# Optimization experiments

Measured on AMD Instinct MI355X. Metric: run time of the kernel, lower is better.

Reference implementation:

```python
import jax, jax.numpy as jnp
import numpy as np

N = 20000
E = 320000
IN_F = 128
HEADS = 8
OUT_F = 32
NEG_SLOPE = 0.2


def setup_inputs() -> dict:
    key = jax.random.key(0)
    k = jax.random.split(key, 8)
    x = jax.random.normal(k[0], (N, IN_F), dtype=jnp.float32)
    edge_index = jax.random.randint(k[1], (2, E), 0, N, dtype=jnp.int32)
    # Linear weights stored torch-style: [out, in]
    scale = 1.0 / np.sqrt(IN_F)
    W = jax.random.normal(k[2], (HEADS * OUT_F, IN_F), dtype=jnp.float32) * scale
    W1 = jax.random.normal(k[3], (HEADS * OUT_F, IN_F), dtype=jnp.float32) * scale
    W2 = jax.random.normal(k[4], (HEADS * OUT_F, IN_F), dtype=jnp.float32) * scale
    att = jax.random.normal(k[5], (1, HEADS, OUT_F), dtype=jnp.float32) * 0.1
    bias = jnp.zeros((HEADS * OUT_F,), dtype=jnp.float32)
    return {"x": x, "edge_index": edge_index, "W": W, "W1": W1, "W2": W2,
            "att": att, "bias": bias}


def reference(x, edge_index, W, W1, W2, att, bias):
    n, heads, out_f = x.shape[0], att.shape[1], att.shape[2]
    src, dst = edge_index[0], edge_index[1]

    # Node projections: [N, H, F]
    h_src = (x @ W1.T).reshape(n, heads, out_f)
    h_dst = (x @ W2.T).reshape(n, heads, out_f)
    values = (x @ W.T).reshape(n, heads, out_f)

    # Edge-wise GATv2 logits: a^T LeakyReLU(W1 h_i + W2 h_j)  -> [E, H]
    att_input = jax.nn.leaky_relu(h_src[src] + h_dst[dst], negative_slope=NEG_SLOPE)
    logits = jnp.einsum('ehf,hf->eh', att_input, att[0])

    # Segment softmax over incoming edges of each dst node (stable).
    seg_max = jax.ops.segment_max(logits, dst, num_segments=n)  # [N, H]
    exp_l = jnp.exp(logits - seg_max[dst])
    denom = jax.ops.segment_sum(exp_l, dst, num_segments=n)     # [N, H]
    weights = exp_l / denom[dst]                                # [E, H]

    # Weighted aggregation of source values into dst nodes.
    weighted = weights[:, :, None] * values[src]                # [E, H, F]
    out = jax.ops.segment_sum(weighted, dst, num_segments=n)    # [N, H, F]

    out = out.reshape(n, heads * out_f) + bias
    return out
```

## Files before the change

kernel.cpp:

```cpp
#include <hip/hip_runtime.h>
#include <math.h>

#define NN 20000
#define EE 320000
#define KF 128
#define HO 256
#define CAP 96

typedef __attribute__((ext_vector_type(8))) short short8;
typedef __attribute__((ext_vector_type(4))) float f32x4;
typedef __attribute__((ext_vector_type(2))) _Float16 half2_t;

static __device__ __forceinline__ unsigned short f2bf(float f) {
    union { float f; unsigned u; } v; v.f = f;
    unsigned u = v.u;
    u += 0x7fffu + ((u >> 16) & 1u);
    return (unsigned short)(u >> 16);
}
static __device__ __forceinline__ unsigned short f2h(float f) {
    _Float16 h = (_Float16)f;
    return __builtin_bit_cast(unsigned short, h);
}
static __device__ __forceinline__ float dot2f(half2_t a, half2_t b, float c) {
#if __has_builtin(__builtin_amdgcn_fdot2)
    return __builtin_amdgcn_fdot2(a, b, c, false);
#else
    return c + (float)a[0] * (float)b[0] + (float)a[1] * (float)b[1];
#endif
}

static __device__ __forceinline__ unsigned f_to_e3m4(float f) {
    const unsigned uf = __builtin_bit_cast(unsigned, f);
    float a = fabsf(f);
    a = fminf(fmaxf(a, 0.03125f), 7.75f);
    const unsigned ua = __builtin_bit_cast(unsigned, a);
    unsigned code = (ua - (122u << 23) + (1u << 18)) >> 19;
    code = (code > 127u) ? 127u : code;
    return ((uf >> 31) << 7) | code;
}
static __device__ __forceinline__ void e3m4x4_to_h2(unsigned w, half2_t& h01, half2_t& h23) {
    const unsigned u01 = __builtin_amdgcn_perm(0u, w, 0x0C010C00u);
    const unsigned u23 = __builtin_amdgcn_perm(0u, w, 0x0C030C02u);
    const unsigned r01 = ((u01 & 0x00800080u) << 8) | (((u01 & 0x007F007Fu) << 6) + 0x28002800u);
    const unsigned r23 = ((u23 & 0x00800080u) << 8) | (((u23 & 0x007F007Fu) << 6) + 0x28002800u);
    h01 = __builtin_bit_cast(half2_t, r01);
    h23 = __builtin_bit_cast(half2_t, r23);
}

__global__ __launch_bounds__(256) void prep_kernel(
    const float* __restrict__ x, const float* __restrict__ W0,
    const float* __restrict__ W1, const float* __restrict__ W2,
    unsigned short* __restrict__ xb, unsigned short* __restrict__ wb,
    int* __restrict__ cursor)
{
    const int b = blockIdx.x;
    const int t = threadIdx.x;
    if (b < 96) {
        const int m = b >> 5;
        const float* __restrict__ Wm = (m == 0) ? W0 : (m == 1) ? W1 : W2;
        int idx = (b & 31) * 1024 + t * 4;
        float4 v = *(const float4*)(Wm + idx);
        ushort4 o;
        o.x = f2bf(v.x); o.y = f2bf(v.y); o.z = f2bf(v.z); o.w = f2bf(v.w);
        *(ushort4*)(wb + (size_t)m * 32768 + idx) = o;
    } else if (b < 2596) {
        size_t i = (size_t)(b - 96) * 1024 + t * 4;
        float4 v = *(const float4*)(x + i);
        ushort4 o;
        o.x = f2bf(v.x); o.y = f2bf(v.y); o.z = f2bf(v.z); o.w = f2bf(v.w);
        *(ushort4*)(xb + i) = o;
    } else {
        int i = (b - 2596) * 256 + t;
        if (i < NN) cursor[i] = 0;
    }
}

__global__ __launch_bounds__(256, 4) void mid_kernel(
    const unsigned short* __restrict__ xb, const unsigned short* __restrict__ wb,
    unsigned short* __restrict__ vb, unsigned char* __restrict__ h8,
    unsigned short* __restrict__ hdst,
    const int* __restrict__ ei, int* __restrict__ cursor, int* __restrict__ csr_src)
{
    const int bid = blockIdx.x;
    if (bid < 1250) {
        const int e = bid * 256 + threadIdx.x;
        if (e < EE) {
            int s = ei[e];
            int d = ei[EE + e];
            int pos = atomicAdd(&cursor[d], 1);
            if (pos < CAP) csr_src[d * CAP + pos] = s;
        }
        return;
    }
    const int pb = bid - 1250;
    const int m  = (pb < 313) ? 0 : (pb < 626) ? 1 : 2;
    const int bx = pb - m * 313;
    const unsigned short* __restrict__ Wm = wb + (size_t)m * 32768;

    const int w    = threadIdx.x >> 6;
    const int lane = threadIdx.x & 63;
    const int lr   = lane & 15;
    const int q    = lane >> 4;
    const int cb   = w * 64;

    short8 Bf[4][4];
#pragma unroll
    for (int nt = 0; nt < 4; ++nt)
#pragma unroll
        for (int ks = 0; ks < 4; ++ks)
            Bf[nt][ks] = *(const short8*)(Wm + (size_t)(cb + nt * 16 + lr) * KF + ks * 32 + q * 8);

    const int rb = bx * 64;

#pragma unroll
    for (int it = 0; it < 4; ++it) {
        const int r0 = rb + it * 16;

        short8 Af[4];
        const int arow = r0 + lr;
#pragma unroll
        for (int ks = 0; ks < 4; ++ks) {
            Af[ks] = (short8){0,0,0,0,0,0,0,0};
            if (arow < NN)
                Af[ks] = *(const short8*)(xb + (size_t)arow * KF + ks * 32 + q * 8);
        }

        f32x4 acc[4];
#pragma unroll
        for (int nt = 0; nt < 4; ++nt) acc[nt] = (f32x4){0.f, 0.f, 0.f, 0.f};

#pragma unroll
        for (int ks = 0; ks < 4; ++ks)
#pragma unroll
            for (int nt = 0; nt < 4; ++nt)
                acc[nt] = __builtin_amdgcn_mfma_f32_16x16x32_bf16(Af[ks], Bf[nt][ks], acc[nt], 0, 0, 0);

#pragma unroll
        for (int nt = 0; nt < 4; ++nt) {
            const int f = cb + nt * 16 + lr;
#pragma unroll
            for (int r = 0; r < 4; ++r) {
                const int row = r0 + q * 4 + r;
                if (row < NN) {
                    const float val = acc[nt][r];
                    if (m == 1)      h8[(size_t)row * 256 + f] = (unsigned char)f_to_e3m4(val);
                    else if (m == 0) vb[(size_t)row * 256 + f] = f2h(val);
                    else             hdst[(size_t)row * 256 + f] = f2h(val);
                }
            }
        }
    }
}

__global__ __launch_bounds__(128) void gat_kernel(
    const unsigned short* __restrict__ vb, const unsigned char* __restrict__ h8,
    const unsigned short* __restrict__ hdst,
    const float* __restrict__ att, const float* __restrict__ bias,
    const int* __restrict__ cursor, const int* __restrict__ csr_src,
    float* __restrict__ out)
{
    const int w    = threadIdx.x >> 6;
    const int d    = blockIdx.x * 2 + w;
    const int lane = threadIdx.x & 63;
    const int col  = lane * 4;

    const float LOG2E = 1.4426950408889634f;
    const float4 av = *(const float4*)(att + col);
    const float s6 = 0.6f * LOG2E, s4 = 0.4f * LOG2E;
    const half2_t a6_01 = { (_Float16)(s6 * av.x), (_Float16)(s6 * av.y) };
    const half2_t a6_23 = { (_Float16)(s6 * av.z), (_Float16)(s6 * av.w) };
    const half2_t a4_01 = { (_Float16)(s4 * av.x), (_Float16)(s4 * av.y) };
    const half2_t a4_23 = { (_Float16)(s4 * av.z), (_Float16)(s4 * av.w) };
    const float4 b4 = *(const float4*)(bias + col);

    const uint2 hdb = *(const uint2*)(hdst + (size_t)d * HO + col);
    const half2_t hd01 = __builtin_bit_cast(half2_t, hdb.x);
    const half2_t hd23 = __builtin_bit_cast(half2_t, hdb.y);

    int deg = cursor[d];
    if (deg > CAP) deg = CAP;

    int sreg = (lane < deg) ? csr_src[d * CAP + lane] : 0;

    float l = 0.f;
    float o0 = 0.f, o1 = 0.f, o2 = 0.f, o3 = 0.f;

#define EDGE_CALC(V, H, VMUL)                                                 \
    {                                                                         \
        half2_t hs01, hs23;                                                   \
        e3m4x4_to_h2(H, hs01, hs23);                                          \
        half2_t z01 = hs01 + hd01;                                            \
        half2_t z23 = hs23 + hd23;                                            \
        const unsigned az01 = __builtin_bit_cast(unsigned, z01) & 0x7FFF7FFFu;\
        const unsigned az23 = __builtin_bit_cast(unsigned, z23) & 0x7FFF7FFFu;\
        float p = dot2f(a6_01, z01,                                           \
                  dot2f(a6_23, z23,                                           \
                  dot2f(a4_01, __builtin_bit_cast(half2_t, az01),             \
                  dot2f(a4_23, __builtin_bit_cast(half2_t, az23), 0.f))));    \
        p += __shfl_xor(p, 1); p += __shfl_xor(p, 2); p += __shfl_xor(p, 4);  \
        const float e = __builtin_amdgcn_exp2f(p) * (VMUL);                   \
        l += e;                                                               \
        const half2_t v01 = __builtin_bit_cast(half2_t, V.x);                 \
        const half2_t v23 = __builtin_bit_cast(half2_t, V.y);                 \
        o0 = fmaf((float)v01[0], e, o0);                                      \
        o1 = fmaf((float)v01[1], e, o1);                                      \
        o2 = fmaf((float)v23[0], e, o2);                                      \
        o3 = fmaf((float)v23[1], e, o3);                                      \
    }

    const int ng = (deg < 64) ? deg : 64;
    for (int i = 0; i < ng; i += 8) {
        float mm[8];
        uint2 V[8];
        unsigned H[8];
#pragma unroll
        for (int u = 0; u < 8; ++u) {
            const int s = __shfl(sreg, i + u);
            mm[u] = (i + u < ng) ? 1.f : 0.f;
            V[u] = *(const uint2*)(vb + (size_t)s * 256 + col);
            H[u] = *(const unsigned*)(h8 + (size_t)s * 256 + col);
        }
#pragma unroll
        for (int u = 0; u < 8; ++u) EDGE_CALC(V[u], H[u], mm[u]);
    }
    for (int j = 64; j < deg; ++j) {
        const int s0 = csr_src[d * CAP + j];
        const uint2 v = *(const uint2*)(vb + (size_t)s0 * 256 + col);
        const unsigned h = *(const unsigned*)(h8 + (size_t)s0 * 256 + col);
        EDGE_CALC(v, h, 1.f);
    }
#undef EDGE_CALC

    const float inv = (deg > 0) ? 1.f / l : 0.f;
    float4 res;
    res.x = fmaf(o0, inv, b4.x);
    res.y = fmaf(o1, inv, b4.y);
    res.z = fmaf(o2, inv, b4.z);
    res.w = fmaf(o3, inv, b4.w);
    *(float4*)(out + (size_t)d * HO + col) = res;
}

extern "C" void kernel_launch(void* const* d_in, const int* in_sizes, int n_in,
                              void* d_out, int out_size, void* d_ws, size_t ws_size,
                              hipStream_t stream) {
    const float* x    = (const float*)d_in[0];
    const int*   ei   = (const int*)d_in[1];
    const float* W0   = (const float*)d_in[2];
    const float* W1   = (const float*)d_in[3];
    const float* W2   = (const float*)d_in[4];
    const float* att  = (const float*)d_in[5];
    const float* bias = (const float*)d_in[6];
    float* out = (float*)d_out;

    char* p = (char*)d_ws;
    unsigned short* vb   = (unsigned short*)p; p += (size_t)NN * HO * 2;
    unsigned short* hdst = (unsigned short*)p; p += (size_t)NN * HO * 2;
    unsigned char*  h8   = (unsigned char*)p;  p += (size_t)NN * HO;
    unsigned short* xb   = (unsigned short*)p; p += (size_t)NN * KF * 2;
    unsigned short* wb   = (unsigned short*)p; p += (size_t)3 * 32768 * 2;
    int* cursor  = (int*)p; p += (size_t)NN * sizeof(int);
    int* csr_src = (int*)p; p += (size_t)NN * CAP * sizeof(int);

    prep_kernel<<<2675, 256, 0, stream>>>(x, W0, W1, W2, xb, wb, cursor);
    mid_kernel<<<2189, 256, 0, stream>>>(xb, wb, vb, h8, hdst, ei, cursor, csr_src);
    gat_kernel<<<NN / 2, 128, 0, stream>>>(vb, h8, hdst, att, bias, cursor, csr_src, out);
}
```

Before: 152.3 us.

## Interleave value and src-projection rows, vectorize CSR build, use readlane

Per-node fp16 values and e3m4 source projections now sit together in one 768-byte row, so each gathered edge touches a single contiguous region instead of two separate arrays. The CSR build handles four edges per thread with int4 loads, which cuts its block count from 1250 to 313. The source-index broadcast uses readlane instead of shfl. Together these aim to reduce gather cache-line traffic and scheduling overhead, at the cost of a 768-byte row stride and more atomics per thread.

```diff
diff --git a/kernel.cpp b/kernel.cpp
--- a/kernel.cpp
+++ b/kernel.cpp
@@ -77,22 +77,34 @@
 
 __global__ __launch_bounds__(256, 4) void mid_kernel(
     const unsigned short* __restrict__ xb, const unsigned short* __restrict__ wb,
-    unsigned short* __restrict__ vb, unsigned char* __restrict__ h8,
-    unsigned short* __restrict__ hdst,
+    unsigned char* __restrict__ hv8, unsigned short* __restrict__ hdst,
     const int* __restrict__ ei, int* __restrict__ cursor, int* __restrict__ csr_src)
 {
     const int bid = blockIdx.x;
-    if (bid < 1250) {
-        const int e = bid * 256 + threadIdx.x;
-        if (e < EE) {
-            int s = ei[e];
-            int d = ei[EE + e];
-            int pos = atomicAdd(&cursor[d], 1);
-            if (pos < CAP) csr_src[d * CAP + pos] = s;
+    if (bid < 313) {
+        const int e0 = (bid * 256 + threadIdx.x) * 4;
+        if (e0 + 3 < EE) {
+            const int4 s4 = *(const int4*)(ei + e0);
+            const int4 d4 = *(const int4*)(ei + EE + e0);
+            const int p0 = atomicAdd(&cursor[d4.x], 1);
+            const int p1 = atomicAdd(&cursor[d4.y], 1);
+            const int p2 = atomicAdd(&cursor[d4.z], 1);
+            const int p3 = atomicAdd(&cursor[d4.w], 1);
+            if (p0 < CAP) csr_src[d4.x * CAP + p0] = s4.x;
+            if (p1 < CAP) csr_src[d4.y * CAP + p1] = s4.y;
+            if (p2 < CAP) csr_src[d4.z * CAP + p2] = s4.z;
+            if (p3 < CAP) csr_src[d4.w * CAP + p3] = s4.w;
+        } else {
+            for (int e = e0; e < EE; ++e) {
+                const int s = ei[e];
+                const int d = ei[EE + e];
+                const int pos = atomicAdd(&cursor[d], 1);
+                if (pos < CAP) csr_src[d * CAP + pos] = s;
+            }
         }
         return;
     }
-    const int pb = bid - 1250;
+    const int pb = bid - 313;
     const int m  = (pb < 313) ? 0 : (pb < 626) ? 1 : 2;
     const int bx = pb - m * 313;
     const unsigned short* __restrict__ Wm = wb + (size_t)m * 32768;
@@ -143,9 +155,12 @@
                 const int row = r0 + q * 4 + r;
                 if (row < NN) {
                     const float val = acc[nt][r];
-                    if (m == 1)      h8[(size_t)row * 256 + f] = (unsigned char)f_to_e3m4(val);
-                    else if (m == 0) vb[(size_t)row * 256 + f] = f2h(val);
-                    else             hdst[(size_t)row * 256 + f] = f2h(val);
+                    if (m == 0)
+                        *(unsigned short*)(hv8 + (size_t)row * 768 + 2 * f) = f2h(val);
+                    else if (m == 1)
+                        hv8[(size_t)row * 768 + 512 + f] = (unsigned char)f_to_e3m4(val);
+                    else
+                        hdst[(size_t)row * 256 + f] = f2h(val);
                 }
             }
         }
@@ -153,8 +168,7 @@
 }
 
 __global__ __launch_bounds__(128) void gat_kernel(
-    const unsigned short* __restrict__ vb, const unsigned char* __restrict__ h8,
-    const unsigned short* __restrict__ hdst,
+    const unsigned char* __restrict__ hv8, const unsigned short* __restrict__ hdst,
     const float* __restrict__ att, const float* __restrict__ bias,
     const int* __restrict__ cursor, const int* __restrict__ csr_src,
     float* __restrict__ out)
@@ -163,6 +177,8 @@
     const int d    = blockIdx.x * 2 + w;
     const int lane = threadIdx.x & 63;
     const int col  = lane * 4;
+    const int vo_v = lane * 8;
+    const int vo_h = 512 + lane * 4;
 
     const float LOG2E = 1.4426950408889634f;
     const float4 av = *(const float4*)(att + col);
@@ -215,18 +231,20 @@
         unsigned H[8];
 #pragma unroll
         for (int u = 0; u < 8; ++u) {
-            const int s = __shfl(sreg, i + u);
+            const int s = __builtin_amdgcn_readlane(sreg, (i + u) & 63);
             mm[u] = (i + u < ng) ? 1.f : 0.f;
-            V[u] = *(const uint2*)(vb + (size_t)s * 256 + col);
-            H[u] = *(const unsigned*)(h8 + (size_t)s * 256 + col);
+            const unsigned char* rp = hv8 + (size_t)s * 768;
+            V[u] = *(const uint2*)(rp + vo_v);
+            H[u] = *(const unsigned*)(rp + vo_h);
         }
 #pragma unroll
         for (int u = 0; u < 8; ++u) EDGE_CALC(V[u], H[u], mm[u]);
     }
     for (int j = 64; j < deg; ++j) {
         const int s0 = csr_src[d * CAP + j];
-        const uint2 v = *(const uint2*)(vb + (size_t)s0 * 256 + col);
-        const unsigned h = *(const unsigned*)(h8 + (size_t)s0 * 256 + col);
+        const unsigned char* rp = hv8 + (size_t)s0 * 768;
+        const uint2 v = *(const uint2*)(rp + vo_v);
+        const unsigned h = *(const unsigned*)(rp + vo_h);
         EDGE_CALC(v, h, 1.f);
     }
 #undef EDGE_CALC
@@ -253,15 +271,14 @@
     float* out = (float*)d_out;
 
     char* p = (char*)d_ws;
-    unsigned short* vb   = (unsigned short*)p; p += (size_t)NN * HO * 2;
+    unsigned char*  hv8  = (unsigned char*)p;  p += (size_t)NN * 768;
     unsigned short* hdst = (unsigned short*)p; p += (size_t)NN * HO * 2;
-    unsigned char*  h8   = (unsigned char*)p;  p += (size_t)NN * HO;
     unsigned short* xb   = (unsigned short*)p; p += (size_t)NN * KF * 2;
     unsigned short* wb   = (unsigned short*)p; p += (size_t)3 * 32768 * 2;
     int* cursor  = (int*)p; p += (size_t)NN * sizeof(int);
     int* csr_src = (int*)p; p += (size_t)NN * CAP * sizeof(int);
 
     prep_kernel<<<2675, 256, 0, stream>>>(x, W0, W1, W2, xb, wb, cursor);
-    mid_kernel<<<2189, 256, 0, stream>>>(xb, wb, vb, h8, hdst, ei, cursor, csr_src);
-    gat_kernel<<<NN / 2, 128, 0, stream>>>(vb, h8, hdst, att, bias, cursor, csr_src, out);
-}
+    mid_kernel<<<1252, 256, 0, stream>>>(xb, wb, hv8, hdst, ei, cursor, csr_src);
+    gat_kernel<<<NN / 2, 128, 0, stream>>>(hv8, hdst, att, bias, cursor, csr_src, out);
+}
```

After: 148.7 us. 2.4% less time.
